# Kernel optimization log

Measured on AMD Instinct MI355X. Metric: run time of the kernel, lower is better.

## Reference

```python
import jax, jax.numpy as jnp
import numpy as np

NUM_HEADS = 8
STRIDE = 1
PAD = 1


def _conv(x, w, stride=STRIDE, pad=PAD):
    return jax.lax.conv_general_dilated(
        x, w, (stride, stride), [(pad, pad), (pad, pad)],
        dimension_numbers=("NCHW", "OIHW", "NCHW"))


def setup_inputs() -> dict:
    key = jax.random.key(0)
    ks = jax.random.split(key, 5)
    B, C, H, W = 8, 64, 56, 56
    nh = NUM_HEADS
    x = jax.random.normal(ks[0], (B, C, H, W), dtype=jnp.float32)
    # Conv weights, small init for numerical stability
    Wq = jax.random.normal(ks[1], (C * nh, C, 3, 3), dtype=jnp.float32) * 0.05
    Wk = jax.random.normal(ks[2], (C * nh, C, 3, 3), dtype=jnp.float32) * 0.05
    Wv = jax.random.normal(ks[3], (C * nh, C, 3, 3), dtype=jnp.float32) * 0.05
    Wu = jax.random.normal(ks[4], (C, C * nh, 1, 1), dtype=jnp.float32) * 0.05
    return {"x": x, "Wq": Wq, "Wk": Wk, "Wv": Wv, "Wu": Wu}


def reference(x, Wq, Wk, Wv, Wu):
    B, C, H, W = x.shape
    nh = NUM_HEADS
    # projections: [B, nh*C, H, W] -> [B, nh, C, H, W] -> [B, C, nh, H, W]
    def proj(w):
        y = _conv(x, w).reshape(B, nh, C, H, W)
        return jnp.transpose(y, (0, 2, 1, 3, 4))
    q = proj(Wq)  # [B, C, nh, H, W]
    k = proj(Wk)
    v = proj(Wv)
    scale = 1.0 / np.sqrt(C * nh).astype(np.float32)
    # contract over heads axis ('n'), attend over channel axis: [B, Cq, H, W, Ck]
    scores = jnp.einsum("bqnhw,bknhw->bqhwk", q, k) * scale
    attn = jax.nn.softmax(scores, axis=-1)
    # attended: [B, Cq, nh, H, W]
    attended = jnp.einsum("bqhwk,bknhw->bqnhw", attn, v)
    out = _conv(attended.reshape(B, C * nh, H, W), Wu, stride=1, pad=0)
    return jax.nn.relu(out)
```

## Files before the change

kernel.cpp:

```cpp
#include <hip/hip_runtime.h>
#include <hip/hip_bf16.h>

#define HW   56
#define CIN  64
#define OC   512
#define NPIX (HW * HW)
#define PEL  ((size_t)8 * NPIX * OC)

typedef unsigned short ushort_t;
typedef __attribute__((ext_vector_type(8))) short short8;
typedef __attribute__((ext_vector_type(4))) float floatx4;
typedef __attribute__((ext_vector_type(16))) float floatx16;

static __device__ __forceinline__ ushort_t f2bf(float f) {
  __hip_bfloat16 h = __float2bfloat16(f);
  return *(ushort_t*)&h;
}

#if __has_builtin(__builtin_amdgcn_exp2f)
#define EXP2F(x) __builtin_amdgcn_exp2f(x)
#else
#define EXP2F(x) exp2f(x)
#endif

__global__ __launch_bounds__(256)
void prep_kernel(const float* __restrict__ x, const float* __restrict__ W0,
                 const float* __restrict__ W1, const float* __restrict__ W2,
                 const float* __restrict__ Wu, ushort_t* __restrict__ xT,
                 ushort_t* __restrict__ Wb, ushort_t* __restrict__ WuP) {
  const int bid = blockIdx.x;
  const int tid = threadIdx.x;

  if (bid < 448) {
    __shared__ ushort_t lx[CIN * HW];
    const int h = bid % HW, b = bid / HW;
    for (int idx = tid; idx < CIN * HW; idx += 256) {
      int c = idx / HW, w = idx - c * HW;
      lx[idx] = f2bf(x[((size_t)(b * CIN + c) * HW + h) * HW + w]);
    }
    __syncthreads();
    ushort_t* dst = xT + ((size_t)(b * HW + h)) * HW * CIN;
    for (int i = tid; i < (CIN * HW) / 4; i += 256) {
      int e0 = i * 4;
      int w = e0 >> 6, c0 = e0 & 63;
      ushort4 o;
      o.x = lx[(c0 + 0) * HW + w];
      o.y = lx[(c0 + 1) * HW + w];
      o.z = lx[(c0 + 2) * HW + w];
      o.w = lx[(c0 + 3) * HW + w];
      ((ushort4*)dst)[i] = o;
    }
  } else if (bid < 832) {
    __shared__ float lw[4 * 576];
    const int u = bid - 448;
    const int sel = u / 128;
    const int jbase = (u % 128) * 4;
    const float* W = sel == 0 ? W0 : (sel == 1 ? W1 : W2);
    ushort_t* Ds = Wb + (size_t)sel * 9 * OC * CIN;

    #pragma unroll
    for (int q = 0; q < 4; ++q) {
      const int j = jbase + q;
      const int src = (sel < 2) ? ((j & 7) * 64 + (j >> 3)) : j;
      for (int i = tid; i < 576; i += 256)
        lw[q * 576 + i] = W[(size_t)src * 576 + i];
    }
    __syncthreads();

    const int q = tid >> 6, cin = tid & 63;
    const int j = jbase + q;
    #pragma unroll
    for (int tap = 0; tap < 9; ++tap)
      Ds[((size_t)tap * OC + j) * CIN + cin] = f2bf(lw[q * 576 + cin * 9 + tap]);
  } else {
    const int el = (bid - 832) * 256 + tid;
    WuP[el] = f2bf(Wu[el]);
  }
}

#define XLS 72
#define XROW (58 * XLS)

__global__ __launch_bounds__(256, 2)
void conv3x3_qkv(const ushort_t* __restrict__ xT, const ushort_t* __restrict__ Wb,
                 ushort_t* __restrict__ yq) {
  __shared__ __align__(16) ushort_t xl[6 * XROW];

  const int tid  = threadIdx.x;
  const int lane = tid & 63;
  const int wv   = tid >> 6;
  const int g    = blockIdx.x;
  const int ob   = blockIdx.y;
  const int b    = blockIdx.z;
  const int h0   = g * 4;
  const int l31  = lane & 31;
  const int khi  = lane >> 5;

  int rowcol[7], rowv[7];
  #pragma unroll
  for (int t = 0; t < 7; ++t) {
    int p = t * 32 + l31;
    int row = p / HW, ww = p - row * HW;
    rowcol[t] = (row * 58 + ww) * XLS;
    rowv[t] = row;
  }

  const ushort_t* wb0 = Wb + ((size_t)(ob * 128 + wv * 32 + l31)) * CIN + khi * 8;

  for (int r = 0; r < 6; ++r) {
    int gh = h0 - 1 + r;
    const int sw = 2 * ((-r) & 3);
    if (gh >= 0 && gh < HW) {
      const uint4* src = (const uint4*)(xT + ((size_t)(b * HW + gh) * HW) * CIN);
      for (int idx = tid; idx < 448; idx += 256) {
        int w = idx >> 3, c8 = idx & 7;
        int col = 1 + w;
        int p8 = (c8 + sw) & 7;
        *(uint4*)&xl[(r * 58 + col) * XLS + p8 * 8] = src[idx];
      }
      if (tid < 16) {
        int col = (tid >> 3) ? 57 : 0, c8 = tid & 7;
        int p8 = (c8 + sw) & 7;
        *(uint4*)&xl[(r * 58 + col) * XLS + p8 * 8] = (uint4){0, 0, 0, 0};
      }
    } else {
      for (int idx = tid; idx < 464; idx += 256) {
        int col = idx >> 3, c8 = idx & 7;
        int p8 = (c8 + sw) & 7;
        *(uint4*)&xl[(r * 58 + col) * XLS + p8 * 8] = (uint4){0, 0, 0, 0};
      }
    }
  }

  short8 BfA[4], BfB[4];
  #pragma unroll
  for (int ck = 0; ck < 4; ++ck)
    BfA[ck] = *(const short8*)(wb0 + ck * 16);

  __syncthreads();

  #pragma unroll 1
  for (int s = 0; s < 3; ++s) {
    floatx16 acc[7];
    #pragma unroll
    for (int t = 0; t < 7; ++t) acc[t] = (floatx16)(0.0f);

    #pragma unroll
    for (int tap = 0; tap < 9; ++tap) {
      const int wtap = s * 9 + tap;
      if (wtap < 26) {
        #pragma unroll
        for (int ck = 0; ck < 4; ++ck)
          BfB[ck] = *(const short8*)(wb0 + (size_t)(wtap + 1) * (OC * CIN) + ck * 16);
      }
      const int kh = tap / 3, kw = tap - kh * 3;
      int baddr[7], b8[7];
      #pragma unroll
      for (int t = 0; t < 7; ++t) {
        baddr[t] = rowcol[t] + (kh * 58 + kw) * XLS;
        b8[t] = khi + 2 * ((-(rowv[t] + kh)) & 3);
      }
      __builtin_amdgcn_s_setprio(1);
      #pragma unroll
      for (int ck = 0; ck < 4; ++ck) {
        #pragma unroll
        for (int t = 0; t < 7; ++t) {
          int chunk = (b8[t] + 2 * ck) & 7;
          short8 af = *(const short8*)&xl[baddr[t] + chunk * 8];
          acc[t] = __builtin_amdgcn_mfma_f32_32x32x16_bf16(af, BfA[ck], acc[t], 0, 0, 0);
        }
      }
      __builtin_amdgcn_s_setprio(0);
      #pragma unroll
      for (int ck = 0; ck < 4; ++ck) BfA[ck] = BfB[ck];
    }

    ushort_t* y = yq + (size_t)s * PEL;
    const int oc = ob * 128 + wv * 32 + l31;
    #pragma unroll
    for (int t = 0; t < 7; ++t) {
      #pragma unroll
      for (int i = 0; i < 16; ++i) {
        int p = t * 32 + (i & 3) + 8 * (i >> 2) + 4 * khi;
        int row = p / HW, ww = p - row * HW;
        size_t pb = ((size_t)((b * HW + h0 + row) * HW + ww)) * OC;
        y[pb + oc] = f2bf(acc[t][i]);
      }
    }
  }
}

#define PST  72
#define A2ST 520

__global__ __launch_bounds__(256, 3)
void attn_kernel(const ushort_t* __restrict__ q, const ushort_t* __restrict__ k,
                 const ushort_t* __restrict__ v, const ushort_t* __restrict__ WuP,
                 float* __restrict__ out) {
  __shared__ __align__(16) ushort_t Pl[4][64 * PST];
  __shared__ __align__(16) ushort_t a2[16 * A2ST];

  const int tid  = threadIdx.x;
  const int lane = tid & 63;
  const int wv   = tid >> 6;
  const int l15  = lane & 15;
  const int quad = lane >> 4;
  const int p0   = blockIdx.x * 16;
  const int b    = blockIdx.y;
  const size_t ibase = ((size_t)b * NPIX + p0) * 512;

  ushort_t* Pw = &Pl[wv][0];
  const float scale2 = 0.063758723f;

  #pragma unroll 1
  for (int i = 0; i < 4; ++i) {
    const int plocal = wv * 4 + i;

    short8 qf[4], kf[4], vf[2];
    {
      const ushort_t* qp = q + ibase + (size_t)plocal * 512;
      const ushort_t* kp = k + ibase + (size_t)plocal * 512;
      const ushort_t* vp = v + ibase + (size_t)plocal * 512;
      #pragma unroll
      for (int nt = 0; nt < 4; ++nt)
        qf[nt] = *(const short8*)(qp + (nt * 16 + l15) * 8);
      #pragma unroll
      for (int mt = 0; mt < 4; ++mt) {
        kf[mt] = (short8){0, 0, 0, 0, 0, 0, 0, 0};
        if (quad == 0) kf[mt] = *(const short8*)(kp + (mt * 16 + l15) * 8);
      }
      #pragma unroll
      for (int ck = 0; ck < 2; ++ck)
        vf[ck] = *(const short8*)(vp + (l15 & 7) * 64 + ck * 32 + quad * 8);
    }

    floatx4 S[4][4];
    #pragma unroll
    for (int mt = 0; mt < 4; ++mt)
      #pragma unroll
      for (int nt = 0; nt < 4; ++nt) S[mt][nt] = (floatx4){0.f, 0.f, 0.f, 0.f};
    __builtin_amdgcn_s_setprio(1);
    #pragma unroll
    for (int mt = 0; mt < 4; ++mt)
      #pragma unroll
      for (int nt = 0; nt < 4; ++nt)
        S[mt][nt] = __builtin_amdgcn_mfma_f32_16x16x32_bf16(kf[mt], qf[nt], S[mt][nt], 0, 0, 0);
    __builtin_amdgcn_s_setprio(0);

    float inv[4];
    #pragma unroll
    for (int nt = 0; nt < 4; ++nt) {
      float e[4][4];
      #pragma unroll
      for (int mt = 0; mt < 4; ++mt)
        #pragma unroll
        for (int r = 0; r < 4; ++r)
          e[mt][r] = EXP2F(S[mt][nt][r] * scale2);
      float sm[4];
      #pragma unroll
      for (int mt = 0; mt < 4; ++mt)
        sm[mt] = (e[mt][0] + e[mt][1]) + (e[mt][2] + e[mt][3]);
      float sum = (sm[0] + sm[1]) + (sm[2] + sm[3]);
      sum += __shfl_xor(sum, 16);
      sum += __shfl_xor(sum, 32);
      inv[nt] = __builtin_amdgcn_rcpf(sum);
      #pragma unroll
      for (int mt = 0; mt < 4; ++mt) {
        ushort4 w4;
        w4.x = f2bf(e[mt][0]);
        w4.y = f2bf(e[mt][1]);
        w4.z = f2bf(e[mt][2]);
        w4.w = f2bf(e[mt][3]);
        *(ushort4*)&Pw[(nt * 16 + l15) * PST + mt * 16 + quad * 4] = w4;
      }
    }

    floatx4 T[4];
    #pragma unroll
    for (int nt = 0; nt < 4; ++nt) T[nt] = (floatx4){0.f, 0.f, 0.f, 0.f};
    __builtin_amdgcn_s_setprio(1);
    #pragma unroll
    for (int ck = 0; ck < 2; ++ck) {
      #pragma unroll
      for (int nt = 0; nt < 4; ++nt) {
        short8 pf = *(const short8*)&Pw[(nt * 16 + l15) * PST + ck * 32 + quad * 8];
        T[nt] = __builtin_amdgcn_mfma_f32_16x16x32_bf16(vf[ck], pf, T[nt], 0, 0, 0);
      }
    }
    __builtin_amdgcn_s_setprio(0);
    if (quad < 2) {
      #pragma unroll
      for (int nt = 0; nt < 4; ++nt) {
        ushort4 w4;
        w4.x = f2bf(T[nt][0] * inv[nt]);
        w4.y = f2bf(T[nt][1] * inv[nt]);
        w4.z = f2bf(T[nt][2] * inv[nt]);
        w4.w = f2bf(T[nt][3] * inv[nt]);
        *(ushort4*)&a2[plocal * A2ST + (nt * 16 + l15) * 8 + quad * 4] = w4;
      }
    }
  }
  __syncthreads();

  floatx4 O = (floatx4){0.f, 0.f, 0.f, 0.f};
  #pragma unroll
  for (int ck = 0; ck < 16; ++ck) {
    short8 aw = *(const short8*)(WuP + (size_t)(wv * 16 + l15) * 512 + ck * 32 + quad * 8);
    short8 bw = *(const short8*)&a2[l15 * A2ST + ck * 32 + quad * 8];
    O = __builtin_amdgcn_mfma_f32_16x16x32_bf16(aw, bw, O, 0, 0, 0);
  }
  #pragma unroll
  for (int r = 0; r < 4; ++r) {
    int co = wv * 16 + quad * 4 + r;
    out[((size_t)b * 64 + co) * NPIX + p0 + l15] = fmaxf(O[r], 0.f);
  }
}

extern "C" void kernel_launch(void* const* d_in, const int* in_sizes, int n_in,
                              void* d_out, int out_size, void* d_ws, size_t ws_size,
                              hipStream_t stream) {
  const float* x  = (const float*)d_in[0];
  const float* Wq = (const float*)d_in[1];
  const float* Wk = (const float*)d_in[2];
  const float* Wv = (const float*)d_in[3];
  const float* Wu = (const float*)d_in[4];
  float* out = (float*)d_out;

  const size_t xT_elems = (size_t)8 * NPIX * CIN;
  const size_t w_elems  = (size_t)9 * OC * CIN;
  const size_t wu_elems = (size_t)64 * 512;
  ushort_t* xT  = (ushort_t*)d_ws;
  ushort_t* Wb  = xT + xT_elems;
  ushort_t* WuP = Wb + 3 * w_elems;
  ushort_t* q   = WuP + wu_elems;
  ushort_t* k   = q + PEL;
  ushort_t* v   = k + PEL;

  prep_kernel<<<960, 256, 0, stream>>>(x, Wq, Wk, Wv, Wu, xT, Wb, WuP);

  dim3 cgrid(14, 4, 8);
  conv3x3_qkv<<<cgrid, 256, 0, stream>>>(xT, Wb, q);

  attn_kernel<<<dim3(NPIX / 16, 8), 256, 0, stream>>>(q, k, v, WuP, out);
}
```

Baseline: 151.6 us.

## Prefetch next pixel's q/k/v and interleave softmax with PV per tile

The attention loop now fully unrolls and software-pipelines the global loads, prefetching the next pixel's q/k/v fragments while the current pixel's MFMAs and softmax run. The P tile scratch is shrunk to one 16-row slab per wave, and the PV MFMA plus normalised writeback are done per nt tile right after its softmax. This is meant to hide global load latency and cut LDS use, which could allow higher occupancy. In exchange it raises register pressure from the double-buffered fragments, and that pressure could limit occupancy under launch_bounds(256,3).

```diff
diff --git a/kernel.cpp b/kernel.cpp
--- a/kernel.cpp
+++ b/kernel.cpp
@@ -197,7 +197,7 @@
 void attn_kernel(const ushort_t* __restrict__ q, const ushort_t* __restrict__ k,
                  const ushort_t* __restrict__ v, const ushort_t* __restrict__ WuP,
                  float* __restrict__ out) {
-  __shared__ __align__(16) ushort_t Pl[4][64 * PST];
+  __shared__ __align__(16) ushort_t Pl[4][16 * PST];
   __shared__ __align__(16) ushort_t a2[16 * A2ST];
 
   const int tid  = threadIdx.x;
@@ -212,27 +212,31 @@
   ushort_t* Pw = &Pl[wv][0];
   const float scale2 = 0.063758723f;
 
-  #pragma unroll 1
+  auto loadpix = [&](int plocal, short8 qf[4], short8 kf[4], short8 vf[2]) {
+    const ushort_t* qp = q + ibase + (size_t)plocal * 512;
+    const ushort_t* kp = k + ibase + (size_t)plocal * 512;
+    const ushort_t* vp = v + ibase + (size_t)plocal * 512;
+    #pragma unroll
+    for (int nt = 0; nt < 4; ++nt)
+      qf[nt] = *(const short8*)(qp + (nt * 16 + l15) * 8);
+    #pragma unroll
+    for (int mt = 0; mt < 4; ++mt) {
+      kf[mt] = (short8){0, 0, 0, 0, 0, 0, 0, 0};
+      if (quad == 0) kf[mt] = *(const short8*)(kp + (mt * 16 + l15) * 8);
+    }
+    #pragma unroll
+    for (int ck = 0; ck < 2; ++ck)
+      vf[ck] = *(const short8*)(vp + (l15 & 7) * 64 + ck * 32 + quad * 8);
+  };
+
+  short8 qf[4], kf[4], vf[2];
+  loadpix(wv * 4, qf, kf, vf);
+
+  #pragma unroll
   for (int i = 0; i < 4; ++i) {
     const int plocal = wv * 4 + i;
-
-    short8 qf[4], kf[4], vf[2];
-    {
-      const ushort_t* qp = q + ibase + (size_t)plocal * 512;
-      const ushort_t* kp = k + ibase + (size_t)plocal * 512;
-      const ushort_t* vp = v + ibase + (size_t)plocal * 512;
-      #pragma unroll
-      for (int nt = 0; nt < 4; ++nt)
-        qf[nt] = *(const short8*)(qp + (nt * 16 + l15) * 8);
-      #pragma unroll
-      for (int mt = 0; mt < 4; ++mt) {
-        kf[mt] = (short8){0, 0, 0, 0, 0, 0, 0, 0};
-        if (quad == 0) kf[mt] = *(const short8*)(kp + (mt * 16 + l15) * 8);
-      }
-      #pragma unroll
-      for (int ck = 0; ck < 2; ++ck)
-        vf[ck] = *(const short8*)(vp + (l15 & 7) * 64 + ck * 32 + quad * 8);
-    }
+    short8 qn[4], kn[4], vn[2];
+    if (i < 3) loadpix(plocal + 1, qn, kn, vn);
 
     floatx4 S[4][4];
     #pragma unroll
@@ -247,7 +251,6 @@
         S[mt][nt] = __builtin_amdgcn_mfma_f32_16x16x32_bf16(kf[mt], qf[nt], S[mt][nt], 0, 0, 0);
     __builtin_amdgcn_s_setprio(0);
 
-    float inv[4];
     #pragma unroll
     for (int nt = 0; nt < 4; ++nt) {
       float e[4][4];
@@ -263,7 +266,8 @@
       float sum = (sm[0] + sm[1]) + (sm[2] + sm[3]);
       sum += __shfl_xor(sum, 16);
       sum += __shfl_xor(sum, 32);
-      inv[nt] = __builtin_amdgcn_rcpf(sum);
+      float inv = __builtin_amdgcn_rcpf(sum);
+
       #pragma unroll
       for (int mt = 0; mt < 4; ++mt) {
         ushort4 w4;
@@ -271,33 +275,32 @@
         w4.y = f2bf(e[mt][1]);
         w4.z = f2bf(e[mt][2]);
         w4.w = f2bf(e[mt][3]);
-        *(ushort4*)&Pw[(nt * 16 + l15) * PST + mt * 16 + quad * 4] = w4;
-      }
-    }
-
-    floatx4 T[4];
-    #pragma unroll
-    for (int nt = 0; nt < 4; ++nt) T[nt] = (floatx4){0.f, 0.f, 0.f, 0.f};
-    __builtin_amdgcn_s_setprio(1);
-    #pragma unroll
-    for (int ck = 0; ck < 2; ++ck) {
-      #pragma unroll
-      for (int nt = 0; nt < 4; ++nt) {
-        short8 pf = *(const short8*)&Pw[(nt * 16 + l15) * PST + ck * 32 + quad * 8];
-        T[nt] = __builtin_amdgcn_mfma_f32_16x16x32_bf16(vf[ck], pf, T[nt], 0, 0, 0);
-      }
-    }
-    __builtin_amdgcn_s_setprio(0);
-    if (quad < 2) {
-      #pragma unroll
-      for (int nt = 0; nt < 4; ++nt) {
+        *(ushort4*)&Pw[l15 * PST + mt * 16 + quad * 4] = w4;
+      }
+
+      floatx4 T = (floatx4){0.f, 0.f, 0.f, 0.f};
+      __builtin_amdgcn_s_setprio(1);
+      #pragma unroll
+      for (int ck = 0; ck < 2; ++ck) {
+        short8 pf = *(const short8*)&Pw[l15 * PST + ck * 32 + quad * 8];
+        T = __builtin_amdgcn_mfma_f32_16x16x32_bf16(vf[ck], pf, T, 0, 0, 0);
+      }
+      __builtin_amdgcn_s_setprio(0);
+      if (quad < 2) {
         ushort4 w4;
-        w4.x = f2bf(T[nt][0] * inv[nt]);
-        w4.y = f2bf(T[nt][1] * inv[nt]);
-        w4.z = f2bf(T[nt][2] * inv[nt]);
-        w4.w = f2bf(T[nt][3] * inv[nt]);
+        w4.x = f2bf(T[0] * inv);
+        w4.y = f2bf(T[1] * inv);
+        w4.z = f2bf(T[2] * inv);
+        w4.w = f2bf(T[3] * inv);
         *(ushort4*)&a2[plocal * A2ST + (nt * 16 + l15) * 8 + quad * 4] = w4;
       }
+    }
+
+    if (i < 3) {
+      #pragma unroll
+      for (int z = 0; z < 4; ++z) { qf[z] = qn[z]; kf[z] = kn[z]; }
+      vf[0] = vn[0];
+      vf[1] = vn[1];
     }
   }
   __syncthreads();
```

Measured after the change: 150.1 us. No clear change (-1.0%).
